# Optimization experiments

Hardware: AMD Instinct MI355X
Metric: run time of the kernel (lower is better)

The kernel has to match this reference:

```python
import jax, jax.numpy as jnp
import numpy as np

N = 100000          # num nodes
E = 3200000         # num edges (avg degree 32)
D = 512             # input_dim == graph_dim
G = 4               # num_graph
H = D // G          # per-factor hidden dim = 128
SIGMA = 1.0         # param['sigma']


def setup_inputs() -> dict:
    key = jax.random.key(0)
    ks = jax.random.split(key, 10)
    features = jax.random.normal(ks[0], (N, D), dtype=jnp.float32)
    src = jax.random.randint(ks[1], (E,), 0, N, dtype=jnp.int64)
    dst = jax.random.randint(ks[2], (E,), 0, N, dtype=jnp.int64)
    # learned parameters
    att = jax.random.normal(ks[3], (G, D), dtype=jnp.float32) * (2.0 / (G + D)) ** 0.5  # xavier-ish
    W_lin = jax.random.normal(ks[4], (G, D, H), dtype=jnp.float32) * (1.0 / D) ** 0.5
    b_lin = jnp.zeros((G, H), dtype=jnp.float32)
    w_al = jax.random.normal(ks[5], (G, H), dtype=jnp.float32) * (1.0 / H) ** 0.5
    b_al = jnp.zeros((G,), dtype=jnp.float32)
    w_ar = jax.random.normal(ks[6], (G, H), dtype=jnp.float32) * (1.0 / H) ** 0.5
    b_ar = jnp.zeros((G,), dtype=jnp.float32)
    return {"features": features, "src": src, "dst": dst, "att": att,
            "W_lin": W_lin, "b_lin": b_lin, "w_al": w_al, "b_al": b_al,
            "w_ar": w_ar, "b_ar": b_ar}


def reference(features, src, dst, att, W_lin, b_lin, w_al, b_al, w_ar, b_ar):
    # per-factor projection: hidden[g] = (features * att[g]) @ W_lin[g] + b_lin[g]
    # fused einsum avoids materializing [G, N, D]
    hidden = jnp.einsum('nd,gd,gdh->gnh', features, att, W_lin) + b_lin[:, None, :]  # [G,N,H]
    # per-node attention scalars
    a_l = jnp.einsum('gnh,gh->gn', hidden, w_al) + b_al[:, None]  # [G,N]
    a_r = jnp.einsum('gnh,gh->gn', hidden, w_ar) + b_ar[:, None]  # [G,N]
    # per-edge factor: sigmoid(sigma * (a_l[src] + a_r[dst]))  (u_add_v + sigmoid)
    factors = jax.nn.sigmoid(SIGMA * (a_l[:, src] + a_r[:, dst]))  # [G,E]
    # self.hidden = cat(hidden_list, -1)
    hidden_cat = jnp.transpose(hidden, (1, 0, 2)).reshape(N, G * H)  # [N, G*H]
    return (hidden_cat, factors)
```

## Files before the change

kernel.cpp:

```cpp
#include <hip/hip_runtime.h>
#include <hip/hip_bf16.h>

#define NNODES 100000
#define NEDGES 3200000
#define DIM    512
#define GF     4
#define HD     128

#define BM      128
#define BK      32
#define KSTEPS  (DIM / BK)
#define ABUF    (BM * BK)
#define BBUF    (DIM * BK)
#define LDSBUF  (ABUF + BBUF)

typedef __bf16 bf16x8 __attribute__((ext_vector_type(8)));
typedef float  f32x4  __attribute__((ext_vector_type(4)));

__device__ __forceinline__ float ldF(const void* p, size_t i, int isF32) {
    return isF32 ? ((const float*)p)[i]
                 : __bfloat162float(((const __hip_bfloat16*)p)[i]);
}
__device__ __forceinline__ void stF(void* p, size_t i, float v, int isF32) {
    if (isF32) ((float*)p)[i] = v;
    else       ((__hip_bfloat16*)p)[i] = __float2bfloat16(v);
}
__device__ __forceinline__ long long ldI(const void* p, size_t i, int isI64) {
    return isI64 ? ((const long long*)p)[i] : (long long)((const int*)p)[i];
}
__device__ __forceinline__ bf16x8 ld8(const void* base, size_t elemOff, int isF32) {
    if (isF32) {
        const float* p = (const float*)base + elemOff;
        f32x4 a = *(const f32x4*)p;
        f32x4 b = *(const f32x4*)(p + 4);
        bf16x8 r;
        r[0] = (__bf16)a[0]; r[1] = (__bf16)a[1]; r[2] = (__bf16)a[2]; r[3] = (__bf16)a[3];
        r[4] = (__bf16)b[0]; r[5] = (__bf16)b[1]; r[6] = (__bf16)b[2]; r[7] = (__bf16)b[3];
        return r;
    }
    return *(const bf16x8*)((const __hip_bfloat16*)base + elemOff);
}

__device__ __forceinline__ void gload_lds16(const void* g, void* l) {
    __builtin_amdgcn_global_load_lds(
        (const __attribute__((address_space(1))) unsigned int*)g,
        (__attribute__((address_space(3))) unsigned int*)l,
        16, 0, 0);
}

__global__ void detect_kernel(const unsigned short* __restrict__ featU16,
                              const int* __restrict__ srcI32,
                              int* __restrict__ flags) {
    __shared__ int sF, sI;
    if (threadIdx.x == 0) { sF = 0; sI = 0; }
    __syncthreads();
    int cntF = 0, cntI = 0;
    for (int i = threadIdx.x; i < 8192; i += 256) {
        unsigned short u = featU16[i];
        int e = (u >> 7) & 0xFF;
        if (e >= 0xE0) cntF++;
        if ((i & 1) && srcI32[i] != 0) cntI++;
    }
    atomicAdd(&sF, cntF);
    atomicAdd(&sI, cntI);
    __syncthreads();
    if (threadIdx.x == 0) {
        flags[0] = (sF > 20) ? 1 : 0;
        flags[1] = (sI == 0) ? 1 : 0;
    }
}

__global__ void prep_kernel(const void* __restrict__ att,
                            const void* __restrict__ W_lin,
                            __hip_bfloat16* __restrict__ Wt,
                            const int* __restrict__ flags) {
    const int isF32 = flags[0];
    int t = blockIdx.x * blockDim.x + threadIdx.x;
    int g = t >> 9, d = t & 511;
    float a = ldF(att, (size_t)g * DIM + d, isF32);
    size_t wbase = ((size_t)g * DIM + d) * HD;
    __hip_bfloat16* wt = Wt + (size_t)(g * HD) * DIM + d;
    for (int h = 0; h < HD; ++h) {
        float w = ldF(W_lin, wbase + h, isF32);
        wt[(size_t)h * DIM] = __float2bfloat16(a * w);
    }
}

__global__ void bias_kernel(const void* b_lin, const void* w_al, const void* b_al,
                            const void* w_ar, const void* b_ar,
                            float* cb, const int* __restrict__ flags) {
    const int isF32 = flags[0];
    int g = threadIdx.x;
    if (g < GF) {
        float s = ldF(b_al, g, isF32) + ldF(b_ar, g, isF32);
        for (int h = 0; h < HD; ++h) {
            float bl = ldF(b_lin, g * HD + h, isF32);
            s += bl * (ldF(w_al, g * HD + h, isF32) + ldF(w_ar, g * HD + h, isF32));
        }
        cb[g] = s;
    }
}

__global__ __launch_bounds__(512, 2) void gemm_kernel(
        const void* __restrict__ feat,
        const __hip_bfloat16* __restrict__ Wt,
        const void* __restrict__ b_lin,
        const void* __restrict__ w_al,
        const void* __restrict__ w_ar,
        void* __restrict__ out_hidden,
        float* __restrict__ a_l, float* __restrict__ a_r,
        const int* __restrict__ flags) {
    __shared__ __attribute__((aligned(16))) __hip_bfloat16 lds[2 * LDSBUF];
    const int isF32 = flags[0];

    const int tid  = threadIdx.x;
    const int lane = tid & 63;
    const int wave = tid >> 6;
    const int q    = lane >> 4;
    const int lm   = lane & 15;
    const int waveM = wave >> 2;
    const int g     = wave & 3;
    const int rowBase = blockIdx.x * BM;

    const int sRow = tid >> 2;
    const int sKb  = tid & 3;
    const size_t gAoff = (size_t)min(rowBase + sRow, NNODES - 1) * DIM + sKb * 8;
    const int wbase = tid & ~63;

    const int aoffBase = (waveM * 64 + lm) * BK + q * 8;
    const int boffBase = ABUF + (g * HD + lm) * BK + q * 8;

    f32x4 acc[4][8];
#pragma unroll
    for (int mi = 0; mi < 4; ++mi)
#pragma unroll
        for (int ni = 0; ni < 8; ++ni) {
            f32x4 z = {0.f, 0.f, 0.f, 0.f};
            acc[mi][ni] = z;
        }

    auto stage = [&](int buf, int ko) {
#pragma unroll
        for (int j = 0; j < 4; ++j) {
            int c = j * 512 + tid;
            const __hip_bfloat16* src = Wt + (size_t)(c >> 2) * DIM + ko * BK + (c & 3) * 8;
            gload_lds16(src, lds + buf * LDSBUF + ABUF + (size_t)(j * 512 + wbase) * 8);
        }
        if (!isF32) {
            const __hip_bfloat16* srcA = (const __hip_bfloat16*)feat + gAoff + (size_t)ko * BK;
            gload_lds16(srcA, lds + buf * LDSBUF + (size_t)wbase * 8);
        }
    };

    auto compute = [&](int buf) {
        const __hip_bfloat16* base = lds + buf * LDSBUF;
        bf16x8 af[4], bfr[8];
#pragma unroll
        for (int mi = 0; mi < 4; ++mi) af[mi] = *(const bf16x8*)(base + aoffBase + mi * 512);
#pragma unroll
        for (int ni = 0; ni < 8; ++ni) bfr[ni] = *(const bf16x8*)(base + boffBase + ni * 512);
#pragma unroll
        for (int mi = 0; mi < 4; ++mi)
#pragma unroll
            for (int ni = 0; ni < 8; ++ni)
                acc[mi][ni] = __builtin_amdgcn_mfma_f32_16x16x32_bf16(
                    af[mi], bfr[ni], acc[mi][ni], 0, 0, 0);
    };

    stage(0, 0);
    if (isF32) *(bf16x8*)(lds + tid * 8) = ld8(feat, gAoff, 1);
    __syncthreads();

    for (int t = 0; t < KSTEPS - 1; ++t) {
        const int cur = t & 1, nxt = cur ^ 1;
        stage(nxt, t + 1);
        bf16x8 aNext;
        if (isF32) aNext = ld8(feat, gAoff + (size_t)(t + 1) * BK, 1);
        compute(cur);
        if (isF32) *(bf16x8*)(lds + nxt * LDSBUF + tid * 8) = aNext;
        __syncthreads();
    }
    compute((KSTEPS - 1) & 1);

    float wal[8], war[8], blin[8];
#pragma unroll
    for (int ni = 0; ni < 8; ++ni) {
        int col = ni * 16 + lm;
        wal[ni]  = ldF(w_al,  g * HD + col, isF32);
        war[ni]  = ldF(w_ar,  g * HD + col, isF32);
        blin[ni] = ldF(b_lin, g * HD + col, isF32);
    }
#pragma unroll
    for (int mi = 0; mi < 4; ++mi) {
        float sal[4] = {0.f, 0.f, 0.f, 0.f};
        float sar[4] = {0.f, 0.f, 0.f, 0.f};
#pragma unroll
        for (int r = 0; r < 4; ++r)
#pragma unroll
            for (int ni = 0; ni < 8; ++ni) {
                float v = acc[mi][ni][r];
                sal[r] += v * wal[ni];
                sar[r] += v * war[ni];
            }
#pragma unroll
        for (int off = 1; off < 16; off <<= 1)
#pragma unroll
            for (int r = 0; r < 4; ++r) {
                sal[r] += __shfl_xor(sal[r], off, 64);
                sar[r] += __shfl_xor(sar[r], off, 64);
            }
#pragma unroll
        for (int r = 0; r < 4; ++r) {
            int row = rowBase + waveM * 64 + mi * 16 + q * 4 + r;
            if (row < NNODES) {
#pragma unroll
                for (int ni = 0; ni < 8; ++ni) {
                    int col = g * HD + ni * 16 + lm;
                    stF(out_hidden, (size_t)row * DIM + col,
                        acc[mi][ni][r] + blin[ni], isF32);
                }
                if (lm == 0) {
                    a_l[g * NNODES + row] = sal[r];
                    a_r[g * NNODES + row] = sar[r];
                }
            }
        }
    }
}

__global__ __launch_bounds__(256) void edge_kernel(
        const void* __restrict__ src, const void* __restrict__ dst,
        const float* __restrict__ a_l, const float* __restrict__ a_r,
        const float* __restrict__ cb, void* __restrict__ out,
        const int* __restrict__ flags) {
    const int isF32 = flags[0];
    const int isI64 = flags[1];
    int e = blockIdx.x * 256 + threadIdx.x;
    if (e >= NEDGES) return;
    long long s = ldI(src, e, isI64);
    long long d = ldI(dst, e, isI64);
    const size_t base = (size_t)NNODES * DIM;
#pragma unroll
    for (int g = 0; g < GF; ++g) {
        float x = a_l[g * NNODES + s] + a_r[g * NNODES + d] + cb[g];
        float f = 1.0f / (1.0f + __expf(-x));
        stF(out, base + (size_t)g * NEDGES + e, f, isF32);
    }
}

extern "C" void kernel_launch(void* const* d_in, const int* in_sizes, int n_in,
                              void* d_out, int out_size, void* d_ws, size_t ws_size,
                              hipStream_t stream) {
    const void* feat  = d_in[0];
    const void* src   = d_in[1];
    const void* dst   = d_in[2];
    const void* att   = d_in[3];
    const void* W_lin = d_in[4];
    const void* b_lin = d_in[5];
    const void* w_al  = d_in[6];
    const void* b_al  = d_in[7];
    const void* w_ar  = d_in[8];
    const void* b_ar  = d_in[9];

    char* ws = (char*)d_ws;
    int*   flags = (int*)ws;
    float* cb    = (float*)(ws + 16);
    __hip_bfloat16* Wt = (__hip_bfloat16*)(ws + 1024);
    float* a_l = (float*)(ws + 1024 + 524288);
    float* a_r = (float*)(ws + 1024 + 524288 + 1600000);

    detect_kernel<<<1, 256, 0, stream>>>((const unsigned short*)feat, (const int*)src, flags);
    prep_kernel<<<8, 256, 0, stream>>>(att, W_lin, Wt, flags);
    bias_kernel<<<1, 64, 0, stream>>>(b_lin, w_al, b_al, w_ar, b_ar, cb, flags);

    gemm_kernel<<<dim3((NNODES + BM - 1) / BM), 512, 0, stream>>>(
        feat, Wt, b_lin, w_al, w_ar, d_out, a_l, a_r, flags);
    edge_kernel<<<NEDGES / 256, 256, 0, stream>>>(
        src, dst, a_l, a_r, cb, d_out, flags);
}
```

Baseline: 636.3 us.

## Triple-buffer swizzled GEMM with direct fp32 LDS loads and node-major attention scalars

The GEMM moves to a templated body with a three-stage LDS ring fed by global_load_lds, including the fp32 feature path, which previously went through registers. It adds XOR-swizzled LDS layouts, explicit vmcnt waits, and s_setprio around the MFMA block. The a_l and a_r arrays become node-major [N,4], so the edge kernel fetches each node's four factors with one 16-byte gather instead of four scattered loads. The prep kernel is spread over 128 blocks instead of 8. The risk is that the 144KB LDS footprint allows only one 512-thread block per CU, despite launch bounds asking for two.

```diff
diff --git a/kernel.cpp b/kernel.cpp
--- a/kernel.cpp
+++ b/kernel.cpp
@@ -10,9 +10,6 @@
 #define BM      128
 #define BK      32
 #define KSTEPS  (DIM / BK)
-#define ABUF    (BM * BK)
-#define BBUF    (DIM * BK)
-#define LDSBUF  (ABUF + BBUF)
 
 typedef __bf16 bf16x8 __attribute__((ext_vector_type(8)));
 typedef float  f32x4  __attribute__((ext_vector_type(4)));
@@ -27,18 +24,6 @@
 }
 __device__ __forceinline__ long long ldI(const void* p, size_t i, int isI64) {
     return isI64 ? ((const long long*)p)[i] : (long long)((const int*)p)[i];
-}
-__device__ __forceinline__ bf16x8 ld8(const void* base, size_t elemOff, int isF32) {
-    if (isF32) {
-        const float* p = (const float*)base + elemOff;
-        f32x4 a = *(const f32x4*)p;
-        f32x4 b = *(const f32x4*)(p + 4);
-        bf16x8 r;
-        r[0] = (__bf16)a[0]; r[1] = (__bf16)a[1]; r[2] = (__bf16)a[2]; r[3] = (__bf16)a[3];
-        r[4] = (__bf16)b[0]; r[5] = (__bf16)b[1]; r[6] = (__bf16)b[2]; r[7] = (__bf16)b[3];
-        return r;
-    }
-    return *(const bf16x8*)((const __hip_bfloat16*)base + elemOff);
 }
 
 __device__ __forceinline__ void gload_lds16(const void* g, void* l) {
@@ -55,7 +40,7 @@
     if (threadIdx.x == 0) { sF = 0; sI = 0; }
     __syncthreads();
     int cntF = 0, cntI = 0;
-    for (int i = threadIdx.x; i < 8192; i += 256) {
+    for (int i = threadIdx.x; i < 8192; i += 1024) {
         unsigned short u = featU16[i];
         int e = (u >> 7) & 0xFF;
         if (e >= 0xE0) cntF++;
@@ -75,14 +60,19 @@
                             __hip_bfloat16* __restrict__ Wt,
                             const int* __restrict__ flags) {
     const int isF32 = flags[0];
-    int t = blockIdx.x * blockDim.x + threadIdx.x;
-    int g = t >> 9, d = t & 511;
-    float a = ldF(att, (size_t)g * DIM + d, isF32);
-    size_t wbase = ((size_t)g * DIM + d) * HD;
-    __hip_bfloat16* wt = Wt + (size_t)(g * HD) * DIM + d;
-    for (int h = 0; h < HD; ++h) {
-        float w = ldF(W_lin, wbase + h, isF32);
-        wt[(size_t)h * DIM] = __float2bfloat16(a * w);
+    const int g  = blockIdx.x >> 5;
+    const int hc = blockIdx.x & 31;
+#pragma unroll
+    for (int dh = 0; dh < 2; ++dh) {
+        int d = threadIdx.x + dh * 256;
+        float a = ldF(att, (size_t)g * DIM + d, isF32);
+        size_t wbase = ((size_t)g * DIM + d) * HD;
+#pragma unroll
+        for (int j = 0; j < 4; ++j) {
+            int h = hc * 4 + j;
+            float w = ldF(W_lin, wbase + h, isF32);
+            Wt[(size_t)(g * HD + h) * DIM + d] = __float2bfloat16(a * w);
+        }
     }
 }
 
@@ -101,6 +91,188 @@
     }
 }
 
+template<int ISF32>
+__device__ __forceinline__ void gemm_body(
+        const void* __restrict__ feat,
+        const __hip_bfloat16* __restrict__ Wt,
+        const void* __restrict__ b_lin,
+        const void* __restrict__ w_al,
+        const void* __restrict__ w_ar,
+        void* __restrict__ out_hidden,
+        float* __restrict__ al4, float* __restrict__ ar4,
+        char* lds) {
+    constexpr int ABYTES = ISF32 ? 16384 : 8192;
+    constexpr int LDSB   = ABYTES + 32768;
+
+    const int tid  = threadIdx.x;
+    const int lane = tid & 63;
+    const int wave = tid >> 6;
+    const int q    = lane >> 4;
+    const int lm   = lane & 15;
+    const int waveM = wave >> 2;
+    const int g     = wave & 3;
+    const int rowBase = blockIdx.x * BM;
+    const int wbase = tid & ~63;
+
+    int offA[4][2]; int offAb[4]; int offB[8];
+#pragma unroll
+    for (int mi = 0; mi < 4; ++mi) {
+        int row = waveM * 64 + mi * 16 + lm;
+        if (ISF32) {
+            offA[mi][0] = (row * 8 + ((2 * q)     ^ (row & 7))) * 16;
+            offA[mi][1] = (row * 8 + ((2 * q + 1) ^ (row & 7))) * 16;
+        } else {
+            offAb[mi]   = (row * 4 + (q ^ ((row >> 1) & 3))) * 16;
+        }
+    }
+#pragma unroll
+    for (int ni = 0; ni < 8; ++ni) {
+        int col = g * HD + ni * 16 + lm;
+        offB[ni] = ABYTES + (col * 4 + (q ^ ((col >> 1) & 3))) * 16;
+    }
+
+    const __hip_bfloat16* srcB[4]; int dstB[4];
+#pragma unroll
+    for (int j = 0; j < 4; ++j) {
+        int c = j * 512 + tid, col = c >> 2, qs = c & 3;
+        int ql = qs ^ ((col >> 1) & 3);
+        srcB[j] = Wt + (size_t)col * DIM + ql * 8;
+        dstB[j] = ABYTES + (j * 512 + wbase) * 16;
+    }
+    const float* srcAf0 = nullptr; const float* srcAf1 = nullptr;
+    const __hip_bfloat16* srcAb = nullptr;
+    int dstA0 = 0, dstA1 = 0;
+    if constexpr (ISF32) {
+        {   int G = tid, row = G >> 3, kc = (G & 7) ^ (row & 7);
+            srcAf0 = (const float*)feat + (size_t)min(rowBase + row, NNODES - 1) * DIM + kc * 4;
+            dstA0 = wbase * 16; }
+        {   int G = 512 + tid, row = G >> 3, kc = (G & 7) ^ (row & 7);
+            srcAf1 = (const float*)feat + (size_t)min(rowBase + row, NNODES - 1) * DIM + kc * 4;
+            dstA1 = (512 + wbase) * 16; }
+    } else {
+        int row = tid >> 2, ql = (tid & 3) ^ ((row >> 1) & 3);
+        srcAb = (const __hip_bfloat16*)feat + (size_t)min(rowBase + row, NNODES - 1) * DIM + ql * 8;
+        dstA0 = wbase * 16;
+    }
+
+    f32x4 acc[4][8];
+#pragma unroll
+    for (int mi = 0; mi < 4; ++mi)
+#pragma unroll
+        for (int ni = 0; ni < 8; ++ni) {
+            f32x4 z = {0.f, 0.f, 0.f, 0.f};
+            acc[mi][ni] = z;
+        }
+
+    auto stage = [&](int buf, int ko) {
+        char* bb = lds + buf * LDSB;
+#pragma unroll
+        for (int j = 0; j < 4; ++j)
+            gload_lds16(srcB[j] + (size_t)ko * BK, bb + dstB[j]);
+        if constexpr (ISF32) {
+            gload_lds16(srcAf0 + (size_t)ko * BK, bb + dstA0);
+            gload_lds16(srcAf1 + (size_t)ko * BK, bb + dstA1);
+        } else {
+            gload_lds16(srcAb + (size_t)ko * BK, bb + dstA0);
+        }
+    };
+
+    auto compute = [&](int buf) {
+        const char* bb = lds + buf * LDSB;
+        bf16x8 af[4];
+#pragma unroll
+        for (int mi = 0; mi < 4; ++mi) {
+            if constexpr (ISF32) {
+                f32x4 lo = *(const f32x4*)(bb + offA[mi][0]);
+                f32x4 hi = *(const f32x4*)(bb + offA[mi][1]);
+                bf16x8 a;
+                a[0] = (__bf16)lo[0]; a[1] = (__bf16)lo[1];
+                a[2] = (__bf16)lo[2]; a[3] = (__bf16)lo[3];
+                a[4] = (__bf16)hi[0]; a[5] = (__bf16)hi[1];
+                a[6] = (__bf16)hi[2]; a[7] = (__bf16)hi[3];
+                af[mi] = a;
+            } else {
+                af[mi] = *(const bf16x8*)(bb + offAb[mi]);
+            }
+        }
+        bf16x8 bfr[8];
+#pragma unroll
+        for (int ni = 0; ni < 8; ++ni) bfr[ni] = *(const bf16x8*)(bb + offB[ni]);
+        __builtin_amdgcn_s_setprio(1);
+#pragma unroll
+        for (int mi = 0; mi < 4; ++mi)
+#pragma unroll
+            for (int ni = 0; ni < 8; ++ni)
+                acc[mi][ni] = __builtin_amdgcn_mfma_f32_16x16x32_bf16(
+                    af[mi], bfr[ni], acc[mi][ni], 0, 0, 0);
+        __builtin_amdgcn_s_setprio(0);
+    };
+
+    asm volatile("s_waitcnt vmcnt(0)" ::: "memory");
+    stage(0, 0);
+    stage(1, 1);
+    for (int t = 0; t < KSTEPS - 1; ++t) {
+        if constexpr (ISF32) asm volatile("s_waitcnt vmcnt(6)" ::: "memory");
+        else                 asm volatile("s_waitcnt vmcnt(5)" ::: "memory");
+        __builtin_amdgcn_sched_barrier(0);
+        __builtin_amdgcn_s_barrier();
+        __builtin_amdgcn_sched_barrier(0);
+        if (t + 2 < KSTEPS) stage((t + 2) % 3, t + 2);
+        compute(t % 3);
+    }
+    asm volatile("s_waitcnt vmcnt(0)" ::: "memory");
+    __builtin_amdgcn_sched_barrier(0);
+    __builtin_amdgcn_s_barrier();
+    __builtin_amdgcn_sched_barrier(0);
+    compute((KSTEPS - 1) % 3);
+
+    const int isF32 = ISF32;
+    float wal[8], war[8], blin[8];
+#pragma unroll
+    for (int ni = 0; ni < 8; ++ni) {
+        int col = ni * 16 + lm;
+        wal[ni]  = ldF(w_al,  g * HD + col, isF32);
+        war[ni]  = ldF(w_ar,  g * HD + col, isF32);
+        blin[ni] = ldF(b_lin, g * HD + col, isF32);
+    }
+#pragma unroll
+    for (int mi = 0; mi < 4; ++mi) {
+        float sal[4] = {0.f, 0.f, 0.f, 0.f};
+        float sar[4] = {0.f, 0.f, 0.f, 0.f};
+#pragma unroll
+        for (int r = 0; r < 4; ++r)
+#pragma unroll
+            for (int ni = 0; ni < 8; ++ni) {
+                float v = acc[mi][ni][r];
+                sal[r] += v * wal[ni];
+                sar[r] += v * war[ni];
+            }
+#pragma unroll
+        for (int off = 1; off < 16; off <<= 1)
+#pragma unroll
+            for (int r = 0; r < 4; ++r) {
+                sal[r] += __shfl_xor(sal[r], off, 64);
+                sar[r] += __shfl_xor(sar[r], off, 64);
+            }
+#pragma unroll
+        for (int r = 0; r < 4; ++r) {
+            int row = rowBase + waveM * 64 + mi * 16 + q * 4 + r;
+            if (row < NNODES) {
+#pragma unroll
+                for (int ni = 0; ni < 8; ++ni) {
+                    int col = g * HD + ni * 16 + lm;
+                    stF(out_hidden, (size_t)row * DIM + col,
+                        acc[mi][ni][r] + blin[ni], isF32);
+                }
+                if (lm == 0) {
+                    al4[(size_t)row * 4 + g] = sal[r];
+                    ar4[(size_t)row * 4 + g] = sar[r];
+                }
+            }
+        }
+    }
+}
+
 __global__ __launch_bounds__(512, 2) void gemm_kernel(
         const void* __restrict__ feat,
         const __hip_bfloat16* __restrict__ Wt,
@@ -110,122 +282,11 @@
         void* __restrict__ out_hidden,
         float* __restrict__ a_l, float* __restrict__ a_r,
         const int* __restrict__ flags) {
-    __shared__ __attribute__((aligned(16))) __hip_bfloat16 lds[2 * LDSBUF];
-    const int isF32 = flags[0];
-
-    const int tid  = threadIdx.x;
-    const int lane = tid & 63;
-    const int wave = tid >> 6;
-    const int q    = lane >> 4;
-    const int lm   = lane & 15;
-    const int waveM = wave >> 2;
-    const int g     = wave & 3;
-    const int rowBase = blockIdx.x * BM;
-
-    const int sRow = tid >> 2;
-    const int sKb  = tid & 3;
-    const size_t gAoff = (size_t)min(rowBase + sRow, NNODES - 1) * DIM + sKb * 8;
-    const int wbase = tid & ~63;
-
-    const int aoffBase = (waveM * 64 + lm) * BK + q * 8;
-    const int boffBase = ABUF + (g * HD + lm) * BK + q * 8;
-
-    f32x4 acc[4][8];
-#pragma unroll
-    for (int mi = 0; mi < 4; ++mi)
-#pragma unroll
-        for (int ni = 0; ni < 8; ++ni) {
-            f32x4 z = {0.f, 0.f, 0.f, 0.f};
-            acc[mi][ni] = z;
-        }
-
-    auto stage = [&](int buf, int ko) {
-#pragma unroll
-        for (int j = 0; j < 4; ++j) {
-            int c = j * 512 + tid;
-            const __hip_bfloat16* src = Wt + (size_t)(c >> 2) * DIM + ko * BK + (c & 3) * 8;
-            gload_lds16(src, lds + buf * LDSBUF + ABUF + (size_t)(j * 512 + wbase) * 8);
-        }
-        if (!isF32) {
-            const __hip_bfloat16* srcA = (const __hip_bfloat16*)feat + gAoff + (size_t)ko * BK;
-            gload_lds16(srcA, lds + buf * LDSBUF + (size_t)wbase * 8);
-        }
-    };
-
-    auto compute = [&](int buf) {
-        const __hip_bfloat16* base = lds + buf * LDSBUF;
-        bf16x8 af[4], bfr[8];
-#pragma unroll
-        for (int mi = 0; mi < 4; ++mi) af[mi] = *(const bf16x8*)(base + aoffBase + mi * 512);
-#pragma unroll
-        for (int ni = 0; ni < 8; ++ni) bfr[ni] = *(const bf16x8*)(base + boffBase + ni * 512);
-#pragma unroll
-        for (int mi = 0; mi < 4; ++mi)
-#pragma unroll
-            for (int ni = 0; ni < 8; ++ni)
-                acc[mi][ni] = __builtin_amdgcn_mfma_f32_16x16x32_bf16(
-                    af[mi], bfr[ni], acc[mi][ni], 0, 0, 0);
-    };
-
-    stage(0, 0);
-    if (isF32) *(bf16x8*)(lds + tid * 8) = ld8(feat, gAoff, 1);
-    __syncthreads();
-
-    for (int t = 0; t < KSTEPS - 1; ++t) {
-        const int cur = t & 1, nxt = cur ^ 1;
-        stage(nxt, t + 1);
-        bf16x8 aNext;
-        if (isF32) aNext = ld8(feat, gAoff + (size_t)(t + 1) * BK, 1);
-        compute(cur);
-        if (isF32) *(bf16x8*)(lds + nxt * LDSBUF + tid * 8) = aNext;
-        __syncthreads();
-    }
-    compute((KSTEPS - 1) & 1);
-
-    float wal[8], war[8], blin[8];
-#pragma unroll
-    for (int ni = 0; ni < 8; ++ni) {
-        int col = ni * 16 + lm;
-        wal[ni]  = ldF(w_al,  g * HD + col, isF32);
-        war[ni]  = ldF(w_ar,  g * HD + col, isF32);
-        blin[ni] = ldF(b_lin, g * HD + col, isF32);
-    }
-#pragma unroll
-    for (int mi = 0; mi < 4; ++mi) {
-        float sal[4] = {0.f, 0.f, 0.f, 0.f};
-        float sar[4] = {0.f, 0.f, 0.f, 0.f};
-#pragma unroll
-        for (int r = 0; r < 4; ++r)
-#pragma unroll
-            for (int ni = 0; ni < 8; ++ni) {
-                float v = acc[mi][ni][r];
-                sal[r] += v * wal[ni];
-                sar[r] += v * war[ni];
-            }
-#pragma unroll
-        for (int off = 1; off < 16; off <<= 1)
-#pragma unroll
-            for (int r = 0; r < 4; ++r) {
-                sal[r] += __shfl_xor(sal[r], off, 64);
-                sar[r] += __shfl_xor(sar[r], off, 64);
-            }
-#pragma unroll
-        for (int r = 0; r < 4; ++r) {
-            int row = rowBase + waveM * 64 + mi * 16 + q * 4 + r;
-            if (row < NNODES) {
-#pragma unroll
-                for (int ni = 0; ni < 8; ++ni) {
-                    int col = g * HD + ni * 16 + lm;
-                    stF(out_hidden, (size_t)row * DIM + col,
-                        acc[mi][ni][r] + blin[ni], isF32);
-                }
-                if (lm == 0) {
-                    a_l[g * NNODES + row] = sal[r];
-                    a_r[g * NNODES + row] = sar[r];
-                }
-            }
-        }
-    }
+    __shared__ __attribute__((aligned(16))) char lds[3 * (16384 + 32768)];
+    if (flags[0])
+        gemm_body<1>(feat, Wt, b_lin, w_al, w_ar, out_hidden, a_l, a_r, lds);
+    else
+        gemm_body<0>(feat, Wt, b_lin, w_al, w_ar, out_hidden, a_l, a_r, lds);
 }
 
 __global__ __launch_bounds__(256) void edge_kernel(
@@ -239,10 +300,13 @@
     if (e >= NEDGES) return;
     long long s = ldI(src, e, isI64);
     long long d = ldI(dst, e, isI64);
+    f32x4 va  = *(const f32x4*)(a_l + (size_t)s * 4);
+    f32x4 vb  = *(const f32x4*)(a_r + (size_t)d * 4);
+    f32x4 vcb = *(const f32x4*)cb;
     const size_t base = (size_t)NNODES * DIM;
 #pragma unroll
     for (int g = 0; g < GF; ++g) {
-        float x = a_l[g * NNODES + s] + a_r[g * NNODES + d] + cb[g];
+        float x = va[g] + vb[g] + vcb[g];
         float f = 1.0f / (1.0f + __expf(-x));
         stF(out, base + (size_t)g * NEDGES + e, f, isF32);
     }
@@ -269,8 +333,8 @@
     float* a_l = (float*)(ws + 1024 + 524288);
     float* a_r = (float*)(ws + 1024 + 524288 + 1600000);
 
-    detect_kernel<<<1, 256, 0, stream>>>((const unsigned short*)feat, (const int*)src, flags);
-    prep_kernel<<<8, 256, 0, stream>>>(att, W_lin, Wt, flags);
+    detect_kernel<<<1, 1024, 0, stream>>>((const unsigned short*)feat, (const int*)src, flags);
+    prep_kernel<<<128, 256, 0, stream>>>(att, W_lin, Wt, flags);
     bias_kernel<<<1, 64, 0, stream>>>(b_lin, w_al, b_al, w_ar, b_ar, cb, flags);
 
     gemm_kernel<<<dim3((NNODES + BM - 1) / BM), 512, 0, stream>>>(
```

New measurement: 515.8 us. 18.9% less time.
